# Performance work log

Hardware: AMD Instinct MI355X
Metric: run time of the kernel (lower is better)

Reference implementation:

```python
import jax, jax.numpy as jnp
import numpy as np

B, T, D_MODEL, D_HEAD = 4, 4096, 512, 64  # batch, token_depth, token_len, d_head
D_K = 64
NEG = -1.0e9  # mask fill value used by the torch module


def setup_inputs() -> dict:
    key = jax.random.key(0)
    kx, kq, kk, kv = jax.random.split(key, 4)
    x = jax.random.normal(kx, (B, T, D_MODEL), dtype=jnp.float32)
    # nn.Linear(token_len, d_head, bias=False) -> weight shape [d_head, token_len]
    Wq = jax.random.normal(kq, (D_HEAD, D_MODEL), dtype=jnp.float32) * 0.02
    Wk = jax.random.normal(kk, (D_HEAD, D_MODEL), dtype=jnp.float32) * 0.02
    Wv = jax.random.normal(kv, (D_HEAD, D_MODEL), dtype=jnp.float32) * 0.02
    return {"x": x, "Wq": Wq, "Wk": Wk, "Wv": Wv}


def reference(x, Wq, Wk, Wv):
    # q/k/v projections: y = x @ W.T  (Linear with bias=False)
    q = jnp.einsum("btd,hd->bth", x, Wq)  # [B,T,D_HEAD]
    k = jnp.einsum("btd,hd->bth", x, Wk)
    v = jnp.einsum("btd,hd->bth", x, Wv)

    scores = jnp.einsum("bth,bsh->bts", q, k)  # [B,T,T]

    # additive causal mask: upper triangle (diagonal=1) filled with -1e9
    t_idx = jnp.arange(T)
    mask = jnp.where(t_idx[None, :] > t_idx[:, None], NEG, 0.0).astype(scores.dtype)
    scores = scores + mask[None, :, :]

    sqrt_dk = jnp.sqrt(jnp.asarray(D_K, dtype=scores.dtype))
    # NOTE: original code applies softmax over dim=1 (the query axis), not -1.
    attn = jax.nn.softmax(scores / sqrt_dk, axis=1)
    out = jnp.einsum("bts,bsh->bth", attn, v)  # [B,T,D_HEAD]
    return out
```

## Files before the change

### kernel.cpp

```cpp
#include <hip/hip_runtime.h>

#define B_ 4
#define T_ 4096
#define DM 512
#define DH 64
#define NSTRIP 32
#define NTRI 528

typedef short short8 __attribute__((ext_vector_type(8)));
typedef short bf16x4 __attribute__((ext_vector_type(4)));
typedef float f32x4 __attribute__((ext_vector_type(4)));
typedef float float8 __attribute__((ext_vector_type(8)));

__device__ inline short f2bf(float f) {
    unsigned u = __float_as_uint(f);
    u += 0x7fffu + ((u >> 16) & 1u);
    return (short)(u >> 16);
}
__device__ inline float bf2f(short s) {
    return __uint_as_float(((unsigned)(unsigned short)s) << 16);
}
__device__ inline short8 cvt8(const float* p) {
    float8 v = *(const float8*)p;
    short8 r;
#pragma unroll
    for (int j = 0; j < 8; j++) r[j] = f2bf(v[j]);
    return r;
}
__device__ inline unsigned cvt_pk_bf16(float a, float b) {
    unsigned r;
    asm("v_cvt_pk_bf16_f32 %0, %1, %2" : "=v"(r) : "v"(a), "v"(b));
    return r;
}
__device__ inline bf16x4 pmask4(f32x4 d, int sbase, int t) {
    float p[4];
#pragma unroll
    for (int r = 0; r < 4; r++) {
        float e = __expf(d[r] * 0.125f);
        p[r] = (sbase + r <= t) ? e : 0.f;
    }
    union { unsigned u[2]; bf16x4 v; } z;
    z.u[0] = cvt_pk_bf16(p[0], p[1]);
    z.u[1] = cvt_pk_bf16(p[2], p[3]);
    return z.v;
}
__device__ inline void tri_decode(int m, int& i, int& j) {
    int ii = (int)((__builtin_sqrtf(8.f * (float)m + 1.f) - 1.f) * 0.5f);
    while ((ii + 1) * (ii + 2) / 2 <= m) ii++;
    while (ii * (ii + 1) / 2 > m) ii--;
    i = ii;
    j = m - ii * (ii + 1) / 2;
}

__global__ __launch_bounds__(256, 4) void k_proj(
    const float* __restrict__ x, const float* __restrict__ Wq,
    const float* __restrict__ Wk, const float* __restrict__ Wv,
    short* __restrict__ qb, short* __restrict__ kb, short* __restrict__ vb,
    float* __restrict__ lsum)
{
    __shared__ short Xs[16 * 72];
    __shared__ short Ws[192 * 72];
    int tid = threadIdx.x;
    int lane = tid & 63, w = tid >> 6;
    int l16 = lane & 15, quad = lane >> 4;
    int b = blockIdx.x >> 8;
    int tile = blockIdx.x & 255;
    int t0 = tile * 16;
    long xbase = ((long)(b * T_ + t0)) * DM;
    int hb = w * 3;

    if (tid < 16) lsum[blockIdx.x * 16 + tid] = 0.f;

    f32x4 acc[3];
#pragma unroll
    for (int i = 0; i < 3; i++) acc[i] = (f32x4)(0.f);

    for (int kc = 0; kc < DM; kc += 64) {
        if (tid < 128) {
            int row = tid >> 3, col = (tid & 7) * 8;
            *(short8*)(Xs + row * 72 + col) = cvt8(x + xbase + (long)row * DM + kc + col);
        }
#pragma unroll
        for (int p = 0; p < 6; p++) {
            int idx = p * 256 + tid;
            int row = idx >> 3, col = (idx & 7) * 8;
            const float* Wsrc = (p < 2) ? Wq : (p < 4) ? Wk : Wv;
            *(short8*)(Ws + row * 72 + col) = cvt8(Wsrc + (long)(row & 63) * DM + kc + col);
        }
        __syncthreads();
#pragma unroll
        for (int ks = 0; ks < 2; ks++) {
            short8 af = *(const short8*)(Xs + l16 * 72 + ks * 32 + quad * 8);
#pragma unroll
            for (int j = 0; j < 3; j++) {
                short8 bf = *(const short8*)(Ws + ((hb + j) * 16 + l16) * 72 + ks * 32 + quad * 8);
                acc[j] = __builtin_amdgcn_mfma_f32_16x16x32_bf16(af, bf, acc[j], 0, 0, 0);
            }
        }
        __syncthreads();
    }
#pragma unroll
    for (int j = 0; j < 3; j++) {
        int hh = hb + j, m = hh >> 2, h4 = hh & 3;
        short* outp = (m == 0) ? qb : (m == 1) ? kb : vb;
#pragma unroll
        for (int r4 = 0; r4 < 4; r4++) {
            int t = t0 + quad * 4 + r4;
            outp[((long)(b * T_ + t)) * DH + h4 * 16 + l16] = f2bf(acc[j][r4]);
        }
    }
}

__global__ __launch_bounds__(256, 6) void k_stats(
    const short* __restrict__ qb, const short* __restrict__ kb,
    float* __restrict__ lsum, float* __restrict__ out)
{
    __shared__ short Qb[128 * 72];
    int tid = threadIdx.x;
    int lane = tid & 63, w = tid >> 6;
    int l16 = lane & 15, quad = lane >> 4;

    if (blockIdx.x < 1024)
        *(f32x4*)(out + ((long)blockIdx.x * 256 + tid) * 4) = (f32x4)(0.f);

    int b = blockIdx.x / NTRI;
    int m = blockIdx.x - b * NTRI;
    int ii, jj; tri_decode(NTRI - 1 - m, ii, jj);
    int i = (NSTRIP - 1) - ii, j = (NSTRIP - 1) - jj;
    int s0blk = i * 128;
    int t0 = j * 128;
    int s0w = s0blk + w * 32;
    long bq = (long)b * T_ * DH;

    const short8* kp0 = (const short8*)(kb + bq + (long)(s0w + l16) * DH + quad * 8);
    short8 a00 = kp0[0], a01 = kp0[4];
    const short8* kp1 = (const short8*)(kb + bq + (long)(s0w + 16 + l16) * DH + quad * 8);
    short8 a10 = kp1[0], a11 = kp1[4];

    float acc0[4] = {0.f, 0.f, 0.f, 0.f};
    float acc1[4] = {0.f, 0.f, 0.f, 0.f};

#pragma unroll
    for (int p = 0; p < 4; p++) {
        int idx = p * 256 + tid;
        int row = idx >> 3, col = idx & 7;
        *(short8*)(Qb + row * 72 + col * 8) =
            *(const short8*)(qb + bq + (long)(t0 + row) * DH + col * 8);
    }
    __syncthreads();
    for (int sub = 0; sub < 8; sub++) {
        int tt = t0 + sub * 16;
        if (tt + 15 >= s0w) {
            short8 b0 = *(const short8*)(Qb + (sub * 16 + l16) * 72 + quad * 8);
            short8 b1 = *(const short8*)(Qb + (sub * 16 + l16) * 72 + 32 + quad * 8);
            int t = tt + l16;
            f32x4 d0 = (f32x4)(0.f);
            d0 = __builtin_amdgcn_mfma_f32_16x16x32_bf16(a00, b0, d0, 0, 0, 0);
            d0 = __builtin_amdgcn_mfma_f32_16x16x32_bf16(a01, b1, d0, 0, 0, 0);
#pragma unroll
            for (int r = 0; r < 4; r++) {
                int s = s0w + quad * 4 + r;
                float p = __expf(d0[r] * 0.125f);
                acc0[r] += (t >= s) ? p : 0.f;
            }
            if (tt + 15 >= s0w + 16) {
                f32x4 d1 = (f32x4)(0.f);
                d1 = __builtin_amdgcn_mfma_f32_16x16x32_bf16(a10, b0, d1, 0, 0, 0);
                d1 = __builtin_amdgcn_mfma_f32_16x16x32_bf16(a11, b1, d1, 0, 0, 0);
#pragma unroll
                for (int r = 0; r < 4; r++) {
                    int s = s0w + 16 + quad * 4 + r;
                    float p = __expf(d1[r] * 0.125f);
                    acc1[r] += (t >= s) ? p : 0.f;
                }
            }
        }
    }
#pragma unroll
    for (int r = 0; r < 4; r++) {
        float v = acc0[r];
        v += __shfl_xor(v, 1, 16); v += __shfl_xor(v, 2, 16);
        v += __shfl_xor(v, 4, 16); v += __shfl_xor(v, 8, 16);
        if (l16 == 0) atomicAdd(&lsum[b * T_ + s0w + quad * 4 + r], v);
        float v1 = acc1[r];
        v1 += __shfl_xor(v1, 1, 16); v1 += __shfl_xor(v1, 2, 16);
        v1 += __shfl_xor(v1, 4, 16); v1 += __shfl_xor(v1, 8, 16);
        if (l16 == 0) atomicAdd(&lsum[b * T_ + s0w + 16 + quad * 4 + r], v1);
    }
}

__global__ __launch_bounds__(256) void k_vt(
    const short* __restrict__ vb, const float* __restrict__ lsum, short* __restrict__ vTc)
{
    int tid = threadIdx.x;
    int b = blockIdx.x >> 6;
    int s0 = (blockIdx.x & 63) * 64;
    int h = tid & 63, g = tid >> 6;
    long vbase = ((long)(b * T_) + s0 + g * 16) * DH + h;
    long lbase = (long)b * T_ + s0 + g * 16;
    short8 lo, hi;
#pragma unroll
    for (int k2 = 0; k2 < 8; k2++) {
        float rl = 1.0f / lsum[lbase + k2];
        lo[k2] = f2bf(bf2f(vb[vbase + (long)k2 * DH]) * rl);
        float rh = 1.0f / lsum[lbase + 8 + k2];
        hi[k2] = f2bf(bf2f(vb[vbase + (long)(8 + k2) * DH]) * rh);
    }
    long ob = ((long)(b * 256 + (s0 >> 4) + g) * 64 + h) * 16;
    *(short8*)(vTc + ob) = lo;
    *(short8*)(vTc + ob + 8) = hi;
}

__global__ __launch_bounds__(256, 6) void k_out(
    const short* __restrict__ qb, const short* __restrict__ kb,
    const short* __restrict__ vTc, float* __restrict__ out)
{
    __shared__ short Kb[128 * 72];
    int tid = threadIdx.x;
    int lane = tid & 63, w = tid >> 6;
    int l16 = lane & 15, quad = lane >> 4;
    int b = blockIdx.x / NTRI;
    int m = blockIdx.x - b * NTRI;
    int i, j; tri_decode(m, i, j);
    int s0 = j * 128;
    int t0w = i * 128 + w * 32;
    long bq = (long)b * T_ * DH;

    const short8* qp0 = (const short8*)(qb + bq + (long)(t0w + l16) * DH + quad * 8);
    short8 q00 = qp0[0], q01 = qp0[4];
    const short8* qp1 = (const short8*)(qb + bq + (long)(t0w + 16 + l16) * DH + quad * 8);
    short8 q10 = qp1[0], q11 = qp1[4];
    const short* vTb = vTc + (long)b * (T_ / 16) * DH * 16;

    f32x4 o0[4], o1[4];
#pragma unroll
    for (int ii = 0; ii < 4; ii++) { o0[ii] = (f32x4)(0.f); o1[ii] = (f32x4)(0.f); }
    int t0 = t0w + l16, t1 = t0 + 16;

#pragma unroll
    for (int p = 0; p < 4; p++) {
        int idx = p * 256 + tid;
        int row = idx >> 3, col = idx & 7;
        *(short8*)(Kb + row * 72 + col * 8) =
            *(const short8*)(kb + bq + (long)(s0 + row) * DH + col * 8);
    }
    __syncthreads();

    for (int sub = 0; sub < 8; sub++) {
        int sc = s0 + sub * 16;
        if (sc > t0w + 31) break;
        short8 a0 = *(const short8*)(Kb + (sub * 16 + l16) * 72 + quad * 8);
        short8 a1 = *(const short8*)(Kb + (sub * 16 + l16) * 72 + 32 + quad * 8);
        const short* vc = vTb + (long)(sc >> 4) * 1024 + quad * 4;
        bf16x4 bv[4];
#pragma unroll
        for (int h4 = 0; h4 < 4; h4++)
            bv[h4] = *(const bf16x4*)(vc + (h4 * 16 + l16) * 16);

        f32x4 d1 = (f32x4)(0.f);
        d1 = __builtin_amdgcn_mfma_f32_16x16x32_bf16(a0, q10, d1, 0, 0, 0);
        d1 = __builtin_amdgcn_mfma_f32_16x16x32_bf16(a1, q11, d1, 0, 0, 0);
        bf16x4 pa1 = pmask4(d1, sc + quad * 4, t1);

        bf16x4 pa0 = (bf16x4)(short)0;
        if (sc <= t0w + 15) {
            f32x4 d0 = (f32x4)(0.f);
            d0 = __builtin_amdgcn_mfma_f32_16x16x32_bf16(a0, q00, d0, 0, 0, 0);
            d0 = __builtin_amdgcn_mfma_f32_16x16x32_bf16(a1, q01, d0, 0, 0, 0);
            pa0 = pmask4(d0, sc + quad * 4, t0);
        }
#pragma unroll
        for (int h4 = 0; h4 < 4; h4++) {
            o1[h4] = __builtin_amdgcn_mfma_f32_16x16x16bf16_1k(pa1, bv[h4], o1[h4], 0, 0, 0);
            o0[h4] = __builtin_amdgcn_mfma_f32_16x16x16bf16_1k(pa0, bv[h4], o0[h4], 0, 0, 0);
        }
    }

#pragma unroll
    for (int h4 = 0; h4 < 4; h4++)
#pragma unroll
        for (int r = 0; r < 4; r++) {
            int t = t0w + quad * 4 + r;
            atomicAdd(&out[bq + (long)t * DH + h4 * 16 + l16], o0[h4][r]);
            atomicAdd(&out[bq + (long)(t + 16) * DH + h4 * 16 + l16], o1[h4][r]);
        }
}

extern "C" void kernel_launch(void* const* d_in, const int* in_sizes, int n_in,
                              void* d_out, int out_size, void* d_ws, size_t ws_size,
                              hipStream_t stream) {
    const float* x  = (const float*)d_in[0];
    const float* Wq = (const float*)d_in[1];
    const float* Wk = (const float*)d_in[2];
    const float* Wv = (const float*)d_in[3];
    float* out = (float*)d_out;

    char* ws = (char*)d_ws;
    short* qb   = (short*)(ws);
    short* kb   = (short*)(ws + (2l << 20));
    short* vb   = (short*)(ws + (4l << 20));
    short* vTc  = (short*)(ws + (6l << 20));
    float* lsum = (float*)(ws + (8l << 20));

    k_proj<<<dim3(B_ * T_ / 16), dim3(256), 0, stream>>>(x, Wq, Wk, Wv, qb, kb, vb, lsum);
    k_stats<<<dim3(B_ * NTRI), dim3(256), 0, stream>>>(qb, kb, lsum, out);
    k_vt<<<dim3(B_ * T_ / 64), dim3(256), 0, stream>>>(vb, lsum, vTc);
    k_out<<<dim3(B_ * NTRI), dim3(256), 0, stream>>>(qb, kb, vTc, out);
}
```

Before: 176.7 us.

## Replace triangular 128x128 tiling with per-16-row strips and in-block reductions

```diff
diff --git a/kernel.cpp b/kernel.cpp
--- a/kernel.cpp
+++ b/kernel.cpp
@@ -4,8 +4,7 @@
 #define T_ 4096
 #define DM 512
 #define DH 64
-#define NSTRIP 32
-#define NTRI 528
+#define NST 256
 
 typedef short short8 __attribute__((ext_vector_type(8)));
 typedef short bf16x4 __attribute__((ext_vector_type(4)));
@@ -44,19 +43,11 @@
     z.u[1] = cvt_pk_bf16(p[2], p[3]);
     return z.v;
 }
-__device__ inline void tri_decode(int m, int& i, int& j) {
-    int ii = (int)((__builtin_sqrtf(8.f * (float)m + 1.f) - 1.f) * 0.5f);
-    while ((ii + 1) * (ii + 2) / 2 <= m) ii++;
-    while (ii * (ii + 1) / 2 > m) ii--;
-    i = ii;
-    j = m - ii * (ii + 1) / 2;
-}
 
 __global__ __launch_bounds__(256, 4) void k_proj(
     const float* __restrict__ x, const float* __restrict__ Wq,
     const float* __restrict__ Wk, const float* __restrict__ Wv,
-    short* __restrict__ qb, short* __restrict__ kb, short* __restrict__ vb,
-    float* __restrict__ lsum)
+    short* __restrict__ qb, short* __restrict__ kb, short* __restrict__ vb)
 {
     __shared__ short Xs[16 * 72];
     __shared__ short Ws[192 * 72];
@@ -69,8 +60,6 @@
     long xbase = ((long)(b * T_ + t0)) * DM;
     int hb = w * 3;
 
-    if (tid < 16) lsum[blockIdx.x * 16 + tid] = 0.f;
-
     f32x4 acc[3];
 #pragma unroll
     for (int i = 0; i < 3; i++) acc[i] = (f32x4)(0.f);
@@ -111,82 +100,53 @@
     }
 }
 
-__global__ __launch_bounds__(256, 6) void k_stats(
-    const short* __restrict__ qb, const short* __restrict__ kb,
-    float* __restrict__ lsum, float* __restrict__ out)
-{
-    __shared__ short Qb[128 * 72];
+__global__ __launch_bounds__(256) void k_stats(
+    const short* __restrict__ qb, const short* __restrict__ kb, float* __restrict__ lsum)
+{
+    __shared__ float partS[64];
     int tid = threadIdx.x;
     int lane = tid & 63, w = tid >> 6;
     int l16 = lane & 15, quad = lane >> 4;
-
-    if (blockIdx.x < 1024)
-        *(f32x4*)(out + ((long)blockIdx.x * 256 + tid) * 4) = (f32x4)(0.f);
-
-    int b = blockIdx.x / NTRI;
-    int m = blockIdx.x - b * NTRI;
-    int ii, jj; tri_decode(NTRI - 1 - m, ii, jj);
-    int i = (NSTRIP - 1) - ii, j = (NSTRIP - 1) - jj;
-    int s0blk = i * 128;
-    int t0 = j * 128;
-    int s0w = s0blk + w * 32;
+    int b = blockIdx.x & 3;
+    int rs = blockIdx.x >> 2;
+    int s0 = rs * 16;
     long bq = (long)b * T_ * DH;
 
-    const short8* kp0 = (const short8*)(kb + bq + (long)(s0w + l16) * DH + quad * 8);
-    short8 a00 = kp0[0], a01 = kp0[4];
-    const short8* kp1 = (const short8*)(kb + bq + (long)(s0w + 16 + l16) * DH + quad * 8);
-    short8 a10 = kp1[0], a11 = kp1[4];
-
-    float acc0[4] = {0.f, 0.f, 0.f, 0.f};
-    float acc1[4] = {0.f, 0.f, 0.f, 0.f};
-
-#pragma unroll
-    for (int p = 0; p < 4; p++) {
-        int idx = p * 256 + tid;
-        int row = idx >> 3, col = idx & 7;
-        *(short8*)(Qb + row * 72 + col * 8) =
-            *(const short8*)(qb + bq + (long)(t0 + row) * DH + col * 8);
-    }
-    __syncthreads();
-    for (int sub = 0; sub < 8; sub++) {
-        int tt = t0 + sub * 16;
-        if (tt + 15 >= s0w) {
-            short8 b0 = *(const short8*)(Qb + (sub * 16 + l16) * 72 + quad * 8);
-            short8 b1 = *(const short8*)(Qb + (sub * 16 + l16) * 72 + 32 + quad * 8);
-            int t = tt + l16;
-            f32x4 d0 = (f32x4)(0.f);
-            d0 = __builtin_amdgcn_mfma_f32_16x16x32_bf16(a00, b0, d0, 0, 0, 0);
-            d0 = __builtin_amdgcn_mfma_f32_16x16x32_bf16(a01, b1, d0, 0, 0, 0);
-#pragma unroll
-            for (int r = 0; r < 4; r++) {
-                int s = s0w + quad * 4 + r;
-                float p = __expf(d0[r] * 0.125f);
-                acc0[r] += (t >= s) ? p : 0.f;
-            }
-            if (tt + 15 >= s0w + 16) {
-                f32x4 d1 = (f32x4)(0.f);
-                d1 = __builtin_amdgcn_mfma_f32_16x16x32_bf16(a10, b0, d1, 0, 0, 0);
-                d1 = __builtin_amdgcn_mfma_f32_16x16x32_bf16(a11, b1, d1, 0, 0, 0);
-#pragma unroll
-                for (int r = 0; r < 4; r++) {
-                    int s = s0w + 16 + quad * 4 + r;
-                    float p = __expf(d1[r] * 0.125f);
-                    acc1[r] += (t >= s) ? p : 0.f;
-                }
-            }
+    const short8* kp = (const short8*)(kb + bq + (long)(s0 + l16) * DH + quad * 8);
+    short8 a0 = kp[0], a1 = kp[4];
+
+    int n = NST - rs;
+    int len = (n + 3) >> 2;
+    int off_hi = (w + 1) * len; if (off_hi > n) off_hi = n;
+    int jlo = rs + w * len;
+    int jhi = rs + off_hi;
+
+    float acc[4] = {0.f, 0.f, 0.f, 0.f};
+    for (int j = jlo; j < jhi; j++) {
+        const short8* qp = (const short8*)(qb + bq + (long)(j * 16 + l16) * DH + quad * 8);
+        short8 q0 = qp[0], q1 = qp[4];
+        f32x4 d = (f32x4)(0.f);
+        d = __builtin_amdgcn_mfma_f32_16x16x32_bf16(a0, q0, d, 0, 0, 0);
+        d = __builtin_amdgcn_mfma_f32_16x16x32_bf16(a1, q1, d, 0, 0, 0);
+        int t = j * 16 + l16;
+#pragma unroll
+        for (int r = 0; r < 4; r++) {
+            int s = s0 + quad * 4 + r;
+            float p = __expf(d[r] * 0.125f);
+            acc[r] += (t >= s) ? p : 0.f;
         }
     }
 #pragma unroll
     for (int r = 0; r < 4; r++) {
-        float v = acc0[r];
+        float v = acc[r];
         v += __shfl_xor(v, 1, 16); v += __shfl_xor(v, 2, 16);
         v += __shfl_xor(v, 4, 16); v += __shfl_xor(v, 8, 16);
-        if (l16 == 0) atomicAdd(&lsum[b * T_ + s0w + quad * 4 + r], v);
-        float v1 = acc1[r];
-        v1 += __shfl_xor(v1, 1, 16); v1 += __shfl_xor(v1, 2, 16);
-        v1 += __shfl_xor(v1, 4, 16); v1 += __shfl_xor(v1, 8, 16);
-        if (l16 == 0) atomicAdd(&lsum[b * T_ + s0w + 16 + quad * 4 + r], v1);
-    }
+        if (l16 == 0) partS[w * 16 + quad * 4 + r] = v;
+    }
+    __syncthreads();
+    if (tid < 16)
+        lsum[b * T_ + s0 + tid] =
+            partS[tid] + partS[16 + tid] + partS[32 + tid] + partS[48 + tid];
 }
 
 __global__ __launch_bounds__(256) void k_vt(
@@ -211,79 +171,67 @@
     *(short8*)(vTc + ob + 8) = hi;
 }
 
-__global__ __launch_bounds__(256, 6) void k_out(
+__global__ __launch_bounds__(256) void k_out(
     const short* __restrict__ qb, const short* __restrict__ kb,
     const short* __restrict__ vTc, float* __restrict__ out)
 {
-    __shared__ short Kb[128 * 72];
+    __shared__ float part[256 * 16];
     int tid = threadIdx.x;
     int lane = tid & 63, w = tid >> 6;
     int l16 = lane & 15, quad = lane >> 4;
-    int b = blockIdx.x / NTRI;
-    int m = blockIdx.x - b * NTRI;
-    int i, j; tri_decode(m, i, j);
-    int s0 = j * 128;
-    int t0w = i * 128 + w * 32;
+    int b = blockIdx.x & 3;
+    int r = (NST - 1) - (blockIdx.x >> 2);
+    int t0 = r * 16;
     long bq = (long)b * T_ * DH;
 
-    const short8* qp0 = (const short8*)(qb + bq + (long)(t0w + l16) * DH + quad * 8);
-    short8 q00 = qp0[0], q01 = qp0[4];
-    const short8* qp1 = (const short8*)(qb + bq + (long)(t0w + 16 + l16) * DH + quad * 8);
-    short8 q10 = qp1[0], q11 = qp1[4];
+    const short8* qp = (const short8*)(qb + bq + (long)(t0 + l16) * DH + quad * 8);
+    short8 q0 = qp[0], q1 = qp[4];
     const short* vTb = vTc + (long)b * (T_ / 16) * DH * 16;
-
-    f32x4 o0[4], o1[4];
-#pragma unroll
-    for (int ii = 0; ii < 4; ii++) { o0[ii] = (f32x4)(0.f); o1[ii] = (f32x4)(0.f); }
-    int t0 = t0w + l16, t1 = t0 + 16;
-
-#pragma unroll
-    for (int p = 0; p < 4; p++) {
-        int idx = p * 256 + tid;
-        int row = idx >> 3, col = idx & 7;
-        *(short8*)(Kb + row * 72 + col * 8) =
-            *(const short8*)(kb + bq + (long)(s0 + row) * DH + col * 8);
-    }
+    int t = t0 + l16;
+
+    int n = r + 1;
+    int len = (n + 3) >> 2;
+    int off_hi = (w + 1) * len; if (off_hi > n) off_hi = n;
+    int jlo = w * len;
+    int jhi = off_hi;
+
+    f32x4 o[4];
+#pragma unroll
+    for (int i = 0; i < 4; i++) o[i] = (f32x4)(0.f);
+
+    for (int j = jlo; j < jhi; j++) {
+        const short8* kp = (const short8*)(kb + bq + (long)(j * 16 + l16) * DH + quad * 8);
+        short8 a0 = kp[0], a1 = kp[4];
+        f32x4 d = (f32x4)(0.f);
+        d = __builtin_amdgcn_mfma_f32_16x16x32_bf16(a0, q0, d, 0, 0, 0);
+        d = __builtin_amdgcn_mfma_f32_16x16x32_bf16(a1, q1, d, 0, 0, 0);
+        bf16x4 pa = pmask4(d, j * 16 + quad * 4, t);
+        const short* vc = vTb + (long)j * 1024 + quad * 4;
+#pragma unroll
+        for (int h4 = 0; h4 < 4; h4++) {
+            bf16x4 bv = *(const bf16x4*)(vc + (h4 * 16 + l16) * 16);
+            o[h4] = __builtin_amdgcn_mfma_f32_16x16x16bf16_1k(pa, bv, o[h4], 0, 0, 0);
+        }
+    }
+
+#pragma unroll
+    for (int h4 = 0; h4 < 4; h4++)
+#pragma unroll
+        for (int rr = 0; rr < 4; rr++)
+            part[tid * 16 + h4 * 4 + rr] = o[h4][rr];
     __syncthreads();
-
-    for (int sub = 0; sub < 8; sub++) {
-        int sc = s0 + sub * 16;
-        if (sc > t0w + 31) break;
-        short8 a0 = *(const short8*)(Kb + (sub * 16 + l16) * 72 + quad * 8);
-        short8 a1 = *(const short8*)(Kb + (sub * 16 + l16) * 72 + 32 + quad * 8);
-        const short* vc = vTb + (long)(sc >> 4) * 1024 + quad * 4;
-        bf16x4 bv[4];
+    if (w == 0) {
 #pragma unroll
         for (int h4 = 0; h4 < 4; h4++)
-            bv[h4] = *(const bf16x4*)(vc + (h4 * 16 + l16) * 16);
-
-        f32x4 d1 = (f32x4)(0.f);
-        d1 = __builtin_amdgcn_mfma_f32_16x16x32_bf16(a0, q10, d1, 0, 0, 0);
-        d1 = __builtin_amdgcn_mfma_f32_16x16x32_bf16(a1, q11, d1, 0, 0, 0);
-        bf16x4 pa1 = pmask4(d1, sc + quad * 4, t1);
-
-        bf16x4 pa0 = (bf16x4)(short)0;
-        if (sc <= t0w + 15) {
-            f32x4 d0 = (f32x4)(0.f);
-            d0 = __builtin_amdgcn_mfma_f32_16x16x32_bf16(a0, q00, d0, 0, 0, 0);
-            d0 = __builtin_amdgcn_mfma_f32_16x16x32_bf16(a1, q01, d0, 0, 0, 0);
-            pa0 = pmask4(d0, sc + quad * 4, t0);
-        }
-#pragma unroll
-        for (int h4 = 0; h4 < 4; h4++) {
-            o1[h4] = __builtin_amdgcn_mfma_f32_16x16x16bf16_1k(pa1, bv[h4], o1[h4], 0, 0, 0);
-            o0[h4] = __builtin_amdgcn_mfma_f32_16x16x16bf16_1k(pa0, bv[h4], o0[h4], 0, 0, 0);
-        }
-    }
-
-#pragma unroll
-    for (int h4 = 0; h4 < 4; h4++)
-#pragma unroll
-        for (int r = 0; r < 4; r++) {
-            int t = t0w + quad * 4 + r;
-            atomicAdd(&out[bq + (long)t * DH + h4 * 16 + l16], o0[h4][r]);
-            atomicAdd(&out[bq + (long)(t + 16) * DH + h4 * 16 + l16], o1[h4][r]);
-        }
+#pragma unroll
+            for (int rr = 0; rr < 4; rr++) {
+                int e = h4 * 4 + rr;
+                float s = part[lane * 16 + e] + part[(64 + lane) * 16 + e]
+                        + part[(128 + lane) * 16 + e] + part[(192 + lane) * 16 + e];
+                int tt = t0 + quad * 4 + rr;
+                out[bq + (long)tt * DH + h4 * 16 + l16] = s;
+            }
+    }
 }
 
 extern "C" void kernel_launch(void* const* d_in, const int* in_sizes, int n_in,
@@ -302,8 +250,8 @@
     short* vTc  = (short*)(ws + (6l << 20));
     float* lsum = (float*)(ws + (8l << 20));
 
-    k_proj<<<dim3(B_ * T_ / 16), dim3(256), 0, stream>>>(x, Wq, Wk, Wv, qb, kb, vb, lsum);
-    k_stats<<<dim3(B_ * NTRI), dim3(256), 0, stream>>>(qb, kb, lsum, out);
+    k_proj<<<dim3(B_ * T_ / 16), dim3(256), 0, stream>>>(x, Wq, Wk, Wv, qb, kb, vb);
+    k_stats<<<dim3(B_ * NST), dim3(256), 0, stream>>>(qb, kb, lsum);
     k_vt<<<dim3(B_ * T_ / 64), dim3(256), 0, stream>>>(vb, lsum, vTc);
-    k_out<<<dim3(B_ * NTRI), dim3(256), 0, stream>>>(qb, kb, vTc, out);
-}
+    k_out<<<dim3(B_ * NST), dim3(256), 0, stream>>>(qb, kb, vTc, out);
+}
```

Result: slower. 190.4 us (+7.8%).
